# Kernel tuning notes

Measured on AMD Instinct MI355X. Metric: run time of the kernel, lower is better.

Reference implementation:

```python
import jax, jax.numpy as jnp
import numpy as np

DIM_Q = 512
DIM_K = 512
DIM_V = 512
NUM_HEADS = 8
LN_EPS = 1e-5


def setup_inputs() -> dict:
    key = jax.random.key(0)
    ks = jax.random.split(key, 12)
    s_q = 1.0 / np.sqrt(DIM_Q)
    s_k = 1.0 / np.sqrt(DIM_K)
    s_v = 1.0 / np.sqrt(DIM_V)
    return {
        "Q": jax.random.normal(ks[0], (8, 1024, DIM_Q), dtype=jnp.float32),
        "K": jax.random.normal(ks[1], (8, 1024, DIM_K), dtype=jnp.float32),
        "Wq": jax.random.uniform(ks[2], (DIM_Q, DIM_V), jnp.float32, -s_q, s_q),
        "bq": jax.random.uniform(ks[3], (DIM_V,), jnp.float32, -s_q, s_q),
        "Wk": jax.random.uniform(ks[4], (DIM_K, DIM_V), jnp.float32, -s_k, s_k),
        "bk": jax.random.uniform(ks[5], (DIM_V,), jnp.float32, -s_k, s_k),
        "Wv": jax.random.uniform(ks[6], (DIM_K, DIM_V), jnp.float32, -s_k, s_k),
        "bv": jax.random.uniform(ks[7], (DIM_V,), jnp.float32, -s_k, s_k),
        "Wo": jax.random.uniform(ks[8], (DIM_V, DIM_V), jnp.float32, -s_v, s_v),
        "bo": jax.random.uniform(ks[9], (DIM_V,), jnp.float32, -s_v, s_v),
        "g0": jnp.ones((DIM_V,), jnp.float32),
        "b0": jnp.zeros((DIM_V,), jnp.float32),
        "g1": jnp.ones((DIM_V,), jnp.float32),
        "b1": jnp.zeros((DIM_V,), jnp.float32),
    }


def _layer_norm(x, gamma, beta):
    mu = jnp.mean(x, axis=-1, keepdims=True)
    var = jnp.var(x, axis=-1, keepdims=True)
    return (x - mu) * jax.lax.rsqrt(var + LN_EPS) * gamma + beta


def reference(Q, K, Wq, bq, Wk, bk, Wv, bv, Wo, bo, g0, b0, g1, b1):
    B, Nq, _ = Q.shape
    Nk = K.shape[1]
    H = NUM_HEADS
    d = DIM_V // H  # head dim

    Qp = Q @ Wq + bq                      # [B, Nq, dim_V]
    Kp = K @ Wk + bk                      # [B, Nk, dim_V]
    Vp = K @ Wv + bv                      # [B, Nk, dim_V]

    Qh = Qp.reshape(B, Nq, H, d)
    Kh = Kp.reshape(B, Nk, H, d)
    Vh = Vp.reshape(B, Nk, H, d)

    scores = jnp.einsum("bqhd,bkhd->bhqk", Qh, Kh) / jnp.sqrt(jnp.float32(d))
    A = jax.nn.softmax(scores, axis=-1)   # [B, H, Nq, Nk]
    Oh = jnp.einsum("bhqk,bkhd->bqhd", A, Vh) + Qh  # residual with projected Q
    O = Oh.reshape(B, Nq, DIM_V)

    O = _layer_norm(O, g0, b0)
    O = O + jax.nn.relu(O @ Wo + bo)
    O = _layer_norm(O, g1, b1)
    return O
```

## Files before the change

kernel.cpp:

```cpp
#include <hip/hip_runtime.h>
#include <math.h>

#define DV 512
#define HD 64
#define NHEADS 8
#define SEQ 1024
#define NBATCH 8
#define MROWS (NBATCH * SEQ)

typedef __bf16 bf16;
typedef __bf16 bf16x8 __attribute__((ext_vector_type(8)));
typedef __bf16 bf16x4 __attribute__((ext_vector_type(4)));
typedef float f32x4 __attribute__((ext_vector_type(4)));

__device__ inline void gload_lds16(const void* g, void* l) {
  __builtin_amdgcn_global_load_lds(
      (const __attribute__((address_space(1))) unsigned int*)g,
      (__attribute__((address_space(3))) unsigned int*)l, 16, 0, 0);
}

__global__ __launch_bounds__(256) void prep_w(
    const float* __restrict__ W0, const float* __restrict__ W1,
    const float* __restrict__ W2, const float* __restrict__ W3,
    bf16* __restrict__ T0, bf16* __restrict__ T1,
    bf16* __restrict__ T2, bf16* __restrict__ T3)
{
  const int z = blockIdx.z;
  const float* W = z == 0 ? W0 : z == 1 ? W1 : z == 2 ? W2 : W3;
  bf16* WT = z == 0 ? T0 : z == 1 ? T1 : z == 2 ? T2 : T3;
  __shared__ float T[64][65];
  const int t = threadIdx.x;
  const int k0 = (blockIdx.x >> 3) * 64, n0 = (blockIdx.x & 7) * 64;
#pragma unroll
  for (int p = 0; p < 4; ++p) {
    int r = p * 16 + (t >> 4), c = (t & 15) * 4;
    float4 v = *(const float4*)&W[(size_t)(k0 + r) * DV + n0 + c];
    T[r][c] = v.x; T[r][c + 1] = v.y; T[r][c + 2] = v.z; T[r][c + 3] = v.w;
  }
  __syncthreads();
#pragma unroll
  for (int p = 0; p < 2; ++p) {
    int n = p * 32 + (t >> 3), kc = (t & 7) * 8;
    bf16x8 o;
#pragma unroll
    for (int j = 0; j < 8; ++j) o[j] = (bf16)T[kc + j][n];
    *(bf16x8*)&WT[(size_t)(n0 + n) * DV + k0 + kc] = o;
  }
}

template<bool AF, bool BF>
__device__ __forceinline__ void proj_core(
    const float* Af, const bf16* Ab, const float* Bf, const bf16* Bb,
    bf16* As, bf16* Bs, int m0, int n0, f32x4 (*acc)[4])
{
  const int tid = threadIdx.x;
  const int lane = tid & 63, w = tid >> 6;
  const int wm = w >> 1, wn = w & 1;
  const int cl = lane & 15, qd = lane >> 4;

  size_t offA[4], offB[4];
  int uOff[4], sOff[4];
#pragma unroll
  for (int t = 0; t < 4; ++t) {
    int S = t * 256 + tid;
    int row = S >> 3, kq = (S & 7) ^ (row & 7);
    offA[t] = (size_t)(m0 + row) * DV + kq * 8;
    offB[t] = (size_t)(n0 + row) * DV + kq * 8;
    uOff[t] = (t * 256 + w * 64) * 8;
    sOff[t] = S * 8;
  }

  float4 ra0[4], ra1[4], rb0[4], rb1[4];

#pragma unroll
  for (int t = 0; t < 4; ++t) {
    if (AF) {
      ra0[t] = *(const float4*)(Af + offA[t]);
      ra1[t] = *(const float4*)(Af + offA[t] + 4);
      bf16x8 o;
      o[0]=(bf16)ra0[t].x; o[1]=(bf16)ra0[t].y; o[2]=(bf16)ra0[t].z; o[3]=(bf16)ra0[t].w;
      o[4]=(bf16)ra1[t].x; o[5]=(bf16)ra1[t].y; o[6]=(bf16)ra1[t].z; o[7]=(bf16)ra1[t].w;
      *(bf16x8*)(As + sOff[t]) = o;
    } else {
      gload_lds16(Ab + offA[t], As + uOff[t]);
    }
    if (BF) {
      rb0[t] = *(const float4*)(Bf + offB[t]);
      rb1[t] = *(const float4*)(Bf + offB[t] + 4);
      bf16x8 o;
      o[0]=(bf16)rb0[t].x; o[1]=(bf16)rb0[t].y; o[2]=(bf16)rb0[t].z; o[3]=(bf16)rb0[t].w;
      o[4]=(bf16)rb1[t].x; o[5]=(bf16)rb1[t].y; o[6]=(bf16)rb1[t].z; o[7]=(bf16)rb1[t].w;
      *(bf16x8*)(Bs + sOff[t]) = o;
    } else {
      gload_lds16(Bb + offB[t], Bs + uOff[t]);
    }
  }

  for (int it = 0; it < 8; ++it) {
    __syncthreads();
    const int cur = it & 1;
    const int nb = (cur ^ 1) * 8192;
    const bool has = (it + 1 < 8);
    const size_t k0n = (size_t)(it + 1) * 64;
    if (has) {
#pragma unroll
      for (int t = 0; t < 4; ++t) {
        if (AF) { ra0[t] = *(const float4*)(Af + k0n + offA[t]);
                  ra1[t] = *(const float4*)(Af + k0n + offA[t] + 4); }
        else    gload_lds16(Ab + k0n + offA[t], As + nb + uOff[t]);
        if (BF) { rb0[t] = *(const float4*)(Bf + k0n + offB[t]);
                  rb1[t] = *(const float4*)(Bf + k0n + offB[t] + 4); }
        else    gload_lds16(Bb + k0n + offB[t], Bs + nb + uOff[t]);
      }
    }
    const bf16* A_ = As + cur * 8192;
    const bf16* B_ = Bs + cur * 8192;
#pragma unroll
    for (int cc = 0; cc < 2; ++cc) {
      bf16x8 af[4], bfr[4];
#pragma unroll
      for (int mi = 0; mi < 4; ++mi) {
        int row = wm * 64 + mi * 16 + cl;
        int slot = row * 8 + ((cc * 4 + qd) ^ (row & 7));
        af[mi] = *(const bf16x8*)(A_ + (size_t)slot * 8);
      }
#pragma unroll
      for (int ni = 0; ni < 4; ++ni) {
        int row = wn * 64 + ni * 16 + cl;
        int slot = row * 8 + ((cc * 4 + qd) ^ (row & 7));
        bfr[ni] = *(const bf16x8*)(B_ + (size_t)slot * 8);
      }
#pragma unroll
      for (int mi = 0; mi < 4; ++mi)
#pragma unroll
        for (int ni = 0; ni < 4; ++ni)
          acc[mi][ni] = __builtin_amdgcn_mfma_f32_16x16x32_bf16(
              af[mi], bfr[ni], acc[mi][ni], 0, 0, 0);
    }
    if (has) {
#pragma unroll
      for (int t = 0; t < 4; ++t) {
        if (AF) {
          bf16x8 o;
          o[0]=(bf16)ra0[t].x; o[1]=(bf16)ra0[t].y; o[2]=(bf16)ra0[t].z; o[3]=(bf16)ra0[t].w;
          o[4]=(bf16)ra1[t].x; o[5]=(bf16)ra1[t].y; o[6]=(bf16)ra1[t].z; o[7]=(bf16)ra1[t].w;
          *(bf16x8*)(As + nb + sOff[t]) = o;
        }
        if (BF) {
          bf16x8 o;
          o[0]=(bf16)rb0[t].x; o[1]=(bf16)rb0[t].y; o[2]=(bf16)rb0[t].z; o[3]=(bf16)rb0[t].w;
          o[4]=(bf16)rb1[t].x; o[5]=(bf16)rb1[t].y; o[6]=(bf16)rb1[t].z; o[7]=(bf16)rb1[t].w;
          *(bf16x8*)(Bs + nb + sOff[t]) = o;
        }
      }
    }
  }
}

__global__ __launch_bounds__(256) void gemm_proj(
    const float* __restrict__ Qf, const float* __restrict__ Kf,
    const bf16* __restrict__ WqT, const bf16* __restrict__ WkT,
    const bf16* __restrict__ WvT,
    const float* __restrict__ bq, const float* __restrict__ bk,
    const float* __restrict__ bv,
    bf16* __restrict__ Qp, bf16* __restrict__ Kp, bf16* __restrict__ VpT)
{
  __shared__ bf16 As[2 * 8192];
  __shared__ bf16 Bs[2 * 8192];
  const int z = blockIdx.z;
  int bx, by, N;
  if (z < 2) { by = blockIdx.x & 63; bx = blockIdx.x >> 6; N = DV; }
  else       { bx = blockIdx.x & 63; by = blockIdx.x >> 6; N = MROWS; }
  const int m0 = by * 128, n0 = bx * 128;

  f32x4 acc[4][4] = {};
  const float* bias;
  bf16* C;
  if (z == 0) { proj_core<true,  false>(Qf, nullptr, nullptr, WqT, As, Bs, m0, n0, acc); bias = bq; C = Qp; }
  else if (z == 1) { proj_core<true,  false>(Kf, nullptr, nullptr, WkT, As, Bs, m0, n0, acc); bias = bk; C = Kp; }
  else { proj_core<false, true>(nullptr, WvT, Kf, nullptr, As, Bs, m0, n0, acc); bias = bv; C = VpT; }

  const int lane = threadIdx.x & 63, w = threadIdx.x >> 6;
  const int wm = w >> 1, wn = w & 1;
  const int cl = lane & 15, qd = lane >> 4;
  float bcol[4] = {0.f, 0.f, 0.f, 0.f};
  if (z < 2)
#pragma unroll
    for (int ni = 0; ni < 4; ++ni) bcol[ni] = bias[n0 + wn * 64 + ni * 16 + cl];
#pragma unroll
  for (int mi = 0; mi < 4; ++mi)
#pragma unroll
    for (int r = 0; r < 4; ++r) {
      int gm = m0 + wm * 64 + mi * 16 + qd * 4 + r;
      float brow = (z == 2) ? bias[gm] : 0.f;
#pragma unroll
      for (int ni = 0; ni < 4; ++ni) {
        int gn = n0 + wn * 64 + ni * 16 + cl;
        float v = acc[mi][ni][r] + (z == 2 ? brow : bcol[ni]);
        C[(size_t)gm * N + gn] = (bf16)v;
      }
    }
}

__global__ __launch_bounds__(256) void attn_mfma(
    const bf16* __restrict__ Qp, const bf16* __restrict__ Kp,
    const bf16* __restrict__ VpT, bf16* __restrict__ Orb)
{
  __shared__ bf16 Ks[2][64 * 64];
  __shared__ bf16 Vs[2][64 * 64];
  __shared__ bf16 Ps[4][32 * 72];

  const int tid = threadIdx.x, lane = tid & 63, w = tid >> 6;
  const int cl = lane & 15, qd = lane >> 4;
  const int bh = blockIdx.x, b = bh >> 3, h = bh & 7;
  const int q0w = blockIdx.y * 128 + w * 32;

  const float SCL = 0.18033688011112042f;
  bf16x8 qa[2][2];
#pragma unroll
  for (int qt = 0; qt < 2; ++qt)
#pragma unroll
    for (int ch = 0; ch < 2; ++ch) {
      bf16x8 v = *(const bf16x8*)(Qp + ((size_t)b * SEQ + q0w + qt * 16 + cl) * DV
                                  + h * HD + ch * 32 + qd * 8);
#pragma unroll
      for (int j = 0; j < 8; ++j) v[j] = (bf16)((float)v[j] * SCL);
      qa[qt][ch] = v;
    }

  f32x4 o[4][2] = {};
  float lrun[2] = {0.f, 0.f};

  const bf16* Kbase = Kp + (size_t)b * SEQ * DV + h * HD;
  const bf16* Vbase = VpT + (size_t)h * HD * MROWS + (size_t)b * SEQ;
  bf16* Pw = &Ps[w][0];

  const int Sa = tid, Sb = 256 + tid;
  const int kRowA = Sa >> 3, kDgA = (Sa & 7) ^ (kRowA & 7);
  const int kRowB = Sb >> 3, kDgB = (Sb & 7) ^ (kRowB & 7);
  const size_t kOffA = (size_t)kRowA * DV + kDgA * 8;
  const size_t kOffB = (size_t)kRowB * DV + kDgB * 8;
  const size_t vOffA = (size_t)kRowA * MROWS + kDgA * 8;
  const size_t vOffB = (size_t)kRowB * MROWS + kDgB * 8;

  gload_lds16(Kbase + kOffA, &Ks[0][(size_t)(w * 64) * 8]);
  gload_lds16(Kbase + kOffB, &Ks[0][(size_t)(256 + w * 64) * 8]);
  gload_lds16(Vbase + vOffA, &Vs[0][(size_t)(w * 64) * 8]);
  gload_lds16(Vbase + vOffB, &Vs[0][(size_t)(256 + w * 64) * 8]);

  for (int it = 0; it < SEQ / 64; ++it) {
    __syncthreads();
    const int cur = it & 1;
    if (it + 1 < SEQ / 64) {
      const size_t kt = (size_t)(it + 1) * 64;
      gload_lds16(Kbase + kt * DV + kOffA, &Ks[cur ^ 1][(size_t)(w * 64) * 8]);
      gload_lds16(Kbase + kt * DV + kOffB, &Ks[cur ^ 1][(size_t)(256 + w * 64) * 8]);
      gload_lds16(Vbase + kt + vOffA, &Vs[cur ^ 1][(size_t)(w * 64) * 8]);
      gload_lds16(Vbase + kt + vOffB, &Vs[cur ^ 1][(size_t)(256 + w * 64) * 8]);
    }
    const bf16* K_ = &Ks[cur][0];
    const bf16* V_ = &Vs[cur][0];

    f32x4 sc[4][2] = {};
#pragma unroll
    for (int ch = 0; ch < 2; ++ch) {
      bf16x8 kf[4];
#pragma unroll
      for (int kt4 = 0; kt4 < 4; ++kt4) {
        int key = kt4 * 16 + cl;
        int slot = key * 8 + ((ch * 4 + qd) ^ (key & 7));
        kf[kt4] = *(const bf16x8*)(K_ + (size_t)slot * 8);
      }
#pragma unroll
      for (int kt4 = 0; kt4 < 4; ++kt4)
#pragma unroll
        for (int qt = 0; qt < 2; ++qt)
          sc[kt4][qt] = __builtin_amdgcn_mfma_f32_16x16x32_bf16(
              kf[kt4], qa[qt][ch], sc[kt4][qt], 0, 0, 0);
    }

#pragma unroll
    for (int qt = 0; qt < 2; ++qt) {
      float sum = 0.f;
#pragma unroll
      for (int kt4 = 0; kt4 < 4; ++kt4) {
        float p0 = __builtin_amdgcn_exp2f(sc[kt4][qt][0]);
        float p1 = __builtin_amdgcn_exp2f(sc[kt4][qt][1]);
        float p2 = __builtin_amdgcn_exp2f(sc[kt4][qt][2]);
        float p3 = __builtin_amdgcn_exp2f(sc[kt4][qt][3]);
        sum += (p0 + p1) + (p2 + p3);
        bf16x4 pk;
        pk[0] = (bf16)p0; pk[1] = (bf16)p1; pk[2] = (bf16)p2; pk[3] = (bf16)p3;
        *(bf16x4*)(Pw + (size_t)(qt * 16 + cl) * 72 + kt4 * 16 + qd * 4) = pk;
      }
      sum += __shfl_xor(sum, 16);
      sum += __shfl_xor(sum, 32);
      lrun[qt] += sum;
    }

#pragma unroll
    for (int kc = 0; kc < 2; ++kc) {
      bf16x8 pb[2];
#pragma unroll
      for (int qt = 0; qt < 2; ++qt)
        pb[qt] = *(const bf16x8*)(Pw + (size_t)(qt * 16 + cl) * 72 + kc * 32 + qd * 8);
#pragma unroll
      for (int dt = 0; dt < 4; ++dt) {
        int d = dt * 16 + cl;
        int slot = d * 8 + ((kc * 4 + qd) ^ (d & 7));
        bf16x8 vf = *(const bf16x8*)(V_ + (size_t)slot * 8);
#pragma unroll
        for (int qt = 0; qt < 2; ++qt)
          o[dt][qt] = __builtin_amdgcn_mfma_f32_16x16x32_bf16(
              vf, pb[qt], o[dt][qt], 0, 0, 0);
      }
    }
  }

#pragma unroll
  for (int qt = 0; qt < 2; ++qt) {
    float inv = 1.f / lrun[qt];
    size_t rowoff = ((size_t)b * SEQ + q0w + qt * 16 + cl) * DV + h * HD;
#pragma unroll
    for (int dt = 0; dt < 4; ++dt) {
      bf16x4 rv = *(const bf16x4*)(Qp + rowoff + dt * 16 + qd * 4);
      bf16x4 st;
      st[0] = (bf16)(o[dt][qt][0] * inv + (float)rv[0]);
      st[1] = (bf16)(o[dt][qt][1] * inv + (float)rv[1]);
      st[2] = (bf16)(o[dt][qt][2] * inv + (float)rv[2]);
      st[3] = (bf16)(o[dt][qt][3] * inv + (float)rv[3]);
      *(bf16x4*)(Orb + rowoff + dt * 16 + qd * 4) = st;
    }
  }
}

__global__ __launch_bounds__(256) void gemm_fused(
    const bf16* __restrict__ Orb, const bf16* __restrict__ WoT,
    const float* __restrict__ bo,
    const float* __restrict__ g0, const float* __restrict__ b0,
    const float* __restrict__ g1, const float* __restrict__ b1,
    float* __restrict__ out)
{
  __shared__ bf16 Bsm[32 * 512];
  __shared__ bf16 As[2][2048 * 8];
  const int tid = threadIdx.x, lane = tid & 63, w = tid >> 6;
  const int cl = lane & 15, qd = lane >> 4;
  const int m0 = blockIdx.x * 32;

  size_t offA[8];
  int uOff[8];
#pragma unroll
  for (int t = 0; t < 8; ++t) {
    int S = t * 256 + tid;
    int frow = S >> 2, kq = (S & 3) ^ ((frow >> 1) & 3);
    offA[t] = (size_t)frow * DV + kq * 8;
    uOff[t] = (t * 256 + w * 64) * 8;
  }

#pragma unroll
  for (int t = 0; t < 8; ++t)
    gload_lds16(WoT + offA[t], As[0] + uOff[t]);

  {
    const int q = tid >> 3, c0 = (tid & 7) * 64;
    const bf16* src = Orb + (size_t)(m0 + q) * DV + c0;
    float x[64];
    float s = 0.f, s2 = 0.f;
#pragma unroll
    for (int j = 0; j < 8; ++j) {
      bf16x8 xv = *(const bf16x8*)(src + j * 8);
#pragma unroll
      for (int e = 0; e < 8; ++e) {
        float f = (float)xv[e];
        x[j * 8 + e] = f; s += f; s2 += f * f;
      }
    }
    s  += __shfl_xor(s, 1);  s  += __shfl_xor(s, 2);  s  += __shfl_xor(s, 4);
    s2 += __shfl_xor(s2, 1); s2 += __shfl_xor(s2, 2); s2 += __shfl_xor(s2, 4);
    float mu = s * (1.f / DV);
    float inv = rsqrtf(s2 * (1.f / DV) - mu * mu + 1e-5f);
#pragma unroll
    for (int j = 0; j < 8; ++j) {
      float4 ga = *(const float4*)(g0 + c0 + j * 8);
      float4 gb = *(const float4*)(g0 + c0 + j * 8 + 4);
      float4 ba = *(const float4*)(b0 + c0 + j * 8);
      float4 bb = *(const float4*)(b0 + c0 + j * 8 + 4);
      bf16x8 o;
      o[0] = (bf16)((x[j*8+0] - mu) * inv * ga.x + ba.x);
      o[1] = (bf16)((x[j*8+1] - mu) * inv * ga.y + ba.y);
      o[2] = (bf16)((x[j*8+2] - mu) * inv * ga.z + ba.z);
      o[3] = (bf16)((x[j*8+3] - mu) * inv * ga.w + ba.w);
      o[4] = (bf16)((x[j*8+4] - mu) * inv * gb.x + bb.x);
      o[5] = (bf16)((x[j*8+5] - mu) * inv * gb.y + bb.y);
      o[6] = (bf16)((x[j*8+6] - mu) * inv * gb.z + bb.z);
      o[7] = (bf16)((x[j*8+7] - mu) * inv * gb.w + bb.w);
      int g = (tid & 7) * 8 + j;
      int slot = q * 64 + (g ^ (q & 7));
      *(bf16x8*)(Bsm + (size_t)slot * 8) = o;
    }
  }

  f32x4 acc[8][2] = {};
  for (int it = 0; it < 16; ++it) {
    __syncthreads();
    const int cur = it & 1;
    if (it + 1 < 16) {
#pragma unroll
      for (int t = 0; t < 8; ++t)
        gload_lds16(WoT + (size_t)(it + 1) * 32 + offA[t], As[cur ^ 1] + uOff[t]);
    }
    bf16x8 bfr[2];
#pragma unroll
    for (int nt = 0; nt < 2; ++nt) {
      int q = nt * 16 + cl;
      int slot = q * 64 + ((it * 4 + qd) ^ (q & 7));
      bfr[nt] = *(const bf16x8*)(Bsm + (size_t)slot * 8);
    }
#pragma unroll
    for (int mt = 0; mt < 8; ++mt) {
      int frow = (w * 8 + mt) * 16 + cl;
      int slot = frow * 4 + (qd ^ ((frow >> 1) & 3));
      bf16x8 af = *(const bf16x8*)(As[cur] + (size_t)slot * 8);
#pragma unroll
      for (int nt = 0; nt < 2; ++nt)
        acc[mt][nt] = __builtin_amdgcn_mfma_f32_16x16x32_bf16(
            af, bfr[nt], acc[mt][nt], 0, 0, 0);
    }
  }

  __syncthreads();
  float* red = (float*)As;
  float y[8][2][4];
  float sy[2], sy2[2];
#pragma unroll
  for (int nt = 0; nt < 2; ++nt) {
    sy[nt] = 0.f; sy2[nt] = 0.f;
    const int q = nt * 16 + cl;
#pragma unroll
    for (int mt = 0; mt < 8; ++mt) {
      const int f0 = (w * 8 + mt) * 16 + qd * 4;
      float4 bov = *(const float4*)(bo + f0);
      int g = f0 >> 3;
      int slot = q * 64 + (g ^ (q & 7));
      bf16x4 rv = *(const bf16x4*)(Bsm + (size_t)slot * 8 + (qd & 1) * 4);
      const float* bp = (const float*)&bov;
#pragma unroll
      for (int r = 0; r < 4; ++r) {
        float v = fmaxf(acc[mt][nt][r] + bp[r], 0.f) + (float)rv[r];
        y[mt][nt][r] = v;
        sy[nt] += v; sy2[nt] += v * v;
      }
    }
    sy[nt]  += __shfl_xor(sy[nt], 16);  sy[nt]  += __shfl_xor(sy[nt], 32);
    sy2[nt] += __shfl_xor(sy2[nt], 16); sy2[nt] += __shfl_xor(sy2[nt], 32);
  }
  if (qd == 0) {
#pragma unroll
    for (int nt = 0; nt < 2; ++nt) {
      int q = nt * 16 + cl;
      red[(q * 4 + w) * 2 + 0] = sy[nt];
      red[(q * 4 + w) * 2 + 1] = sy2[nt];
    }
  }
  __syncthreads();
#pragma unroll
  for (int nt = 0; nt < 2; ++nt) {
    const int q = nt * 16 + cl;
    float s = 0.f, s2 = 0.f;
#pragma unroll
    for (int ww = 0; ww < 4; ++ww) {
      s  += red[(q * 4 + ww) * 2 + 0];
      s2 += red[(q * 4 + ww) * 2 + 1];
    }
    float mu1 = s * (1.f / DV);
    float inv1 = rsqrtf(s2 * (1.f / DV) - mu1 * mu1 + 1e-5f);
    size_t rowoff = (size_t)(m0 + q) * DV;
#pragma unroll
    for (int mt = 0; mt < 8; ++mt) {
      const int f0 = (w * 8 + mt) * 16 + qd * 4;
      float4 gv = *(const float4*)(g1 + f0);
      float4 bv = *(const float4*)(b1 + f0);
      float4 ov;
      ov.x = (y[mt][nt][0] - mu1) * inv1 * gv.x + bv.x;
      ov.y = (y[mt][nt][1] - mu1) * inv1 * gv.y + bv.y;
      ov.z = (y[mt][nt][2] - mu1) * inv1 * gv.z + bv.z;
      ov.w = (y[mt][nt][3] - mu1) * inv1 * gv.w + bv.w;
      *(float4*)(out + rowoff + f0) = ov;
    }
  }
}

extern "C" void kernel_launch(void* const* d_in, const int* in_sizes, int n_in,
                              void* d_out, int out_size, void* d_ws, size_t ws_size,
                              hipStream_t stream)
{
  const float* Q  = (const float*)d_in[0];
  const float* Kf = (const float*)d_in[1];
  const float* Wq = (const float*)d_in[2];
  const float* bq = (const float*)d_in[3];
  const float* Wk = (const float*)d_in[4];
  const float* bk = (const float*)d_in[5];
  const float* Wv = (const float*)d_in[6];
  const float* bv = (const float*)d_in[7];
  const float* Wo = (const float*)d_in[8];
  const float* bo = (const float*)d_in[9];
  const float* g0 = (const float*)d_in[10];
  const float* b0 = (const float*)d_in[11];
  const float* g1 = (const float*)d_in[12];
  const float* b1 = (const float*)d_in[13];
  float* out = (float*)d_out;

  const size_t MB = 1ull << 20;
  char* W = (char*)d_ws;
  bf16* Orb = (bf16*)(W + 0);
  bf16* Qp  = (bf16*)(W + 8 * MB);
  bf16* Kp  = (bf16*)(W + 16 * MB);
  bf16* VpT = (bf16*)(W + 24 * MB);
  bf16* WqT = (bf16*)(W + 32 * MB);
  bf16* WkT = (bf16*)(W + 32 * MB + 512 * 1024);
  bf16* WvT = (bf16*)(W + 33 * MB);
  bf16* WoT = (bf16*)(W + 33 * MB + 512 * 1024);

  dim3 blk(256);
  prep_w<<<dim3(64, 1, 4), blk, 0, stream>>>(Wq, Wk, Wv, Wo, WqT, WkT, WvT, WoT);
  gemm_proj<<<dim3(256, 1, 3), blk, 0, stream>>>(
      Q, Kf, WqT, WkT, WvT, bq, bk, bv, Qp, Kp, VpT);
  attn_mfma<<<dim3(NBATCH * NHEADS, SEQ / 128), blk, 0, stream>>>(Qp, Kp, VpT, Orb);
  gemm_fused<<<dim3(MROWS / 32), blk, 0, stream>>>(
      Orb, WoT, bo, g0, b0, g1, b1, out);
}
```

Measured before the change: 185.2 us.

## Load GEMM operands directly from global into registers, bypassing LDS staging

The projection GEMM and the output-projection GEMM no longer stage A/B tiles through double-buffered LDS with barriers. Each lane instead loads its MFMA fragments straight from global memory into registers, prefetching the next K slice one step ahead. This removes LDS traffic and per-iteration __syncthreads, and lets the fused LN kernel keep only a small reduction buffer in shared memory. The cost is that operands are no longer shared across waves, so each wave re-reads overlapping rows from global/L2 with less coalesced access.

After: 225.3 us. +21.6%, slower.

```diff
diff --git a/kernel.cpp b/kernel.cpp
--- a/kernel.cpp
+++ b/kernel.cpp
@@ -17,6 +17,13 @@
   __builtin_amdgcn_global_load_lds(
       (const __attribute__((address_space(1))) unsigned int*)g,
       (__attribute__((address_space(3))) unsigned int*)l, 16, 0, 0);
+}
+
+__device__ __forceinline__ bf16x8 cvt8(float4 a, float4 b) {
+  bf16x8 o;
+  o[0] = (bf16)a.x; o[1] = (bf16)a.y; o[2] = (bf16)a.z; o[3] = (bf16)a.w;
+  o[4] = (bf16)b.x; o[5] = (bf16)b.y; o[6] = (bf16)b.z; o[7] = (bf16)b.w;
+  return o;
 }
 
 __global__ __launch_bounds__(256) void prep_w(
@@ -48,115 +55,6 @@
   }
 }
 
-template<bool AF, bool BF>
-__device__ __forceinline__ void proj_core(
-    const float* Af, const bf16* Ab, const float* Bf, const bf16* Bb,
-    bf16* As, bf16* Bs, int m0, int n0, f32x4 (*acc)[4])
-{
-  const int tid = threadIdx.x;
-  const int lane = tid & 63, w = tid >> 6;
-  const int wm = w >> 1, wn = w & 1;
-  const int cl = lane & 15, qd = lane >> 4;
-
-  size_t offA[4], offB[4];
-  int uOff[4], sOff[4];
-#pragma unroll
-  for (int t = 0; t < 4; ++t) {
-    int S = t * 256 + tid;
-    int row = S >> 3, kq = (S & 7) ^ (row & 7);
-    offA[t] = (size_t)(m0 + row) * DV + kq * 8;
-    offB[t] = (size_t)(n0 + row) * DV + kq * 8;
-    uOff[t] = (t * 256 + w * 64) * 8;
-    sOff[t] = S * 8;
-  }
-
-  float4 ra0[4], ra1[4], rb0[4], rb1[4];
-
-#pragma unroll
-  for (int t = 0; t < 4; ++t) {
-    if (AF) {
-      ra0[t] = *(const float4*)(Af + offA[t]);
-      ra1[t] = *(const float4*)(Af + offA[t] + 4);
-      bf16x8 o;
-      o[0]=(bf16)ra0[t].x; o[1]=(bf16)ra0[t].y; o[2]=(bf16)ra0[t].z; o[3]=(bf16)ra0[t].w;
-      o[4]=(bf16)ra1[t].x; o[5]=(bf16)ra1[t].y; o[6]=(bf16)ra1[t].z; o[7]=(bf16)ra1[t].w;
-      *(bf16x8*)(As + sOff[t]) = o;
-    } else {
-      gload_lds16(Ab + offA[t], As + uOff[t]);
-    }
-    if (BF) {
-      rb0[t] = *(const float4*)(Bf + offB[t]);
-      rb1[t] = *(const float4*)(Bf + offB[t] + 4);
-      bf16x8 o;
-      o[0]=(bf16)rb0[t].x; o[1]=(bf16)rb0[t].y; o[2]=(bf16)rb0[t].z; o[3]=(bf16)rb0[t].w;
-      o[4]=(bf16)rb1[t].x; o[5]=(bf16)rb1[t].y; o[6]=(bf16)rb1[t].z; o[7]=(bf16)rb1[t].w;
-      *(bf16x8*)(Bs + sOff[t]) = o;
-    } else {
-      gload_lds16(Bb + offB[t], Bs + uOff[t]);
-    }
-  }
-
-  for (int it = 0; it < 8; ++it) {
-    __syncthreads();
-    const int cur = it & 1;
-    const int nb = (cur ^ 1) * 8192;
-    const bool has = (it + 1 < 8);
-    const size_t k0n = (size_t)(it + 1) * 64;
-    if (has) {
-#pragma unroll
-      for (int t = 0; t < 4; ++t) {
-        if (AF) { ra0[t] = *(const float4*)(Af + k0n + offA[t]);
-                  ra1[t] = *(const float4*)(Af + k0n + offA[t] + 4); }
-        else    gload_lds16(Ab + k0n + offA[t], As + nb + uOff[t]);
-        if (BF) { rb0[t] = *(const float4*)(Bf + k0n + offB[t]);
-                  rb1[t] = *(const float4*)(Bf + k0n + offB[t] + 4); }
-        else    gload_lds16(Bb + k0n + offB[t], Bs + nb + uOff[t]);
-      }
-    }
-    const bf16* A_ = As + cur * 8192;
-    const bf16* B_ = Bs + cur * 8192;
-#pragma unroll
-    for (int cc = 0; cc < 2; ++cc) {
-      bf16x8 af[4], bfr[4];
-#pragma unroll
-      for (int mi = 0; mi < 4; ++mi) {
-        int row = wm * 64 + mi * 16 + cl;
-        int slot = row * 8 + ((cc * 4 + qd) ^ (row & 7));
-        af[mi] = *(const bf16x8*)(A_ + (size_t)slot * 8);
-      }
-#pragma unroll
-      for (int ni = 0; ni < 4; ++ni) {
-        int row = wn * 64 + ni * 16 + cl;
-        int slot = row * 8 + ((cc * 4 + qd) ^ (row & 7));
-        bfr[ni] = *(const bf16x8*)(B_ + (size_t)slot * 8);
-      }
-#pragma unroll
-      for (int mi = 0; mi < 4; ++mi)
-#pragma unroll
-        for (int ni = 0; ni < 4; ++ni)
-          acc[mi][ni] = __builtin_amdgcn_mfma_f32_16x16x32_bf16(
-              af[mi], bfr[ni], acc[mi][ni], 0, 0, 0);
-    }
-    if (has) {
-#pragma unroll
-      for (int t = 0; t < 4; ++t) {
-        if (AF) {
-          bf16x8 o;
-          o[0]=(bf16)ra0[t].x; o[1]=(bf16)ra0[t].y; o[2]=(bf16)ra0[t].z; o[3]=(bf16)ra0[t].w;
-          o[4]=(bf16)ra1[t].x; o[5]=(bf16)ra1[t].y; o[6]=(bf16)ra1[t].z; o[7]=(bf16)ra1[t].w;
-          *(bf16x8*)(As + nb + sOff[t]) = o;
-        }
-        if (BF) {
-          bf16x8 o;
-          o[0]=(bf16)rb0[t].x; o[1]=(bf16)rb0[t].y; o[2]=(bf16)rb0[t].z; o[3]=(bf16)rb0[t].w;
-          o[4]=(bf16)rb1[t].x; o[5]=(bf16)rb1[t].y; o[6]=(bf16)rb1[t].z; o[7]=(bf16)rb1[t].w;
-          *(bf16x8*)(Bs + nb + sOff[t]) = o;
-        }
-      }
-    }
-  }
-}
-
 __global__ __launch_bounds__(256) void gemm_proj(
     const float* __restrict__ Qf, const float* __restrict__ Kf,
     const bf16* __restrict__ WqT, const bf16* __restrict__ WkT,
@@ -165,24 +63,117 @@
     const float* __restrict__ bv,
     bf16* __restrict__ Qp, bf16* __restrict__ Kp, bf16* __restrict__ VpT)
 {
-  __shared__ bf16 As[2 * 8192];
-  __shared__ bf16 Bs[2 * 8192];
   const int z = blockIdx.z;
   int bx, by, N;
   if (z < 2) { by = blockIdx.x & 63; bx = blockIdx.x >> 6; N = DV; }
   else       { bx = blockIdx.x & 63; by = blockIdx.x >> 6; N = MROWS; }
   const int m0 = by * 128, n0 = bx * 128;
-
-  f32x4 acc[4][4] = {};
-  const float* bias;
-  bf16* C;
-  if (z == 0) { proj_core<true,  false>(Qf, nullptr, nullptr, WqT, As, Bs, m0, n0, acc); bias = bq; C = Qp; }
-  else if (z == 1) { proj_core<true,  false>(Kf, nullptr, nullptr, WkT, As, Bs, m0, n0, acc); bias = bk; C = Kp; }
-  else { proj_core<false, true>(nullptr, WvT, Kf, nullptr, As, Bs, m0, n0, acc); bias = bv; C = VpT; }
-
   const int lane = threadIdx.x & 63, w = threadIdx.x >> 6;
   const int wm = w >> 1, wn = w & 1;
   const int cl = lane & 15, qd = lane >> 4;
+
+  f32x4 acc[4][4] = {};
+
+  if (z < 2) {
+    const float* A = z ? Kf : Qf;
+    const bf16*  B = z ? WkT : WqT;
+    const float* Ap[4];
+    const bf16* Bp[4];
+#pragma unroll
+    for (int mi = 0; mi < 4; ++mi)
+      Ap[mi] = A + (size_t)(m0 + wm * 64 + mi * 16 + cl) * DV + qd * 8;
+#pragma unroll
+    for (int ni = 0; ni < 4; ++ni)
+      Bp[ni] = B + (size_t)(n0 + wn * 64 + ni * 16 + cl) * DV + qd * 8;
+
+    float4 fa[4][2]; bf16x8 cb[4];
+#pragma unroll
+    for (int mi = 0; mi < 4; ++mi) {
+      fa[mi][0] = *(const float4*)Ap[mi];
+      fa[mi][1] = *(const float4*)(Ap[mi] + 4);
+    }
+#pragma unroll
+    for (int ni = 0; ni < 4; ++ni) cb[ni] = *(const bf16x8*)Bp[ni];
+
+    for (int it = 0; it < 16; ++it) {
+      float4 na[4][2]; bf16x8 nb[4];
+      if (it + 1 < 16) {
+        const int k = (it + 1) * 32;
+#pragma unroll
+        for (int mi = 0; mi < 4; ++mi) {
+          na[mi][0] = *(const float4*)(Ap[mi] + k);
+          na[mi][1] = *(const float4*)(Ap[mi] + k + 4);
+        }
+#pragma unroll
+        for (int ni = 0; ni < 4; ++ni) nb[ni] = *(const bf16x8*)(Bp[ni] + k);
+      }
+      bf16x8 af[4];
+#pragma unroll
+      for (int mi = 0; mi < 4; ++mi) af[mi] = cvt8(fa[mi][0], fa[mi][1]);
+#pragma unroll
+      for (int mi = 0; mi < 4; ++mi)
+#pragma unroll
+        for (int ni = 0; ni < 4; ++ni)
+          acc[mi][ni] = __builtin_amdgcn_mfma_f32_16x16x32_bf16(
+              af[mi], cb[ni], acc[mi][ni], 0, 0, 0);
+      if (it + 1 < 16) {
+#pragma unroll
+        for (int mi = 0; mi < 4; ++mi) { fa[mi][0] = na[mi][0]; fa[mi][1] = na[mi][1]; }
+#pragma unroll
+        for (int ni = 0; ni < 4; ++ni) cb[ni] = nb[ni];
+      }
+    }
+  } else {
+    const bf16* Ap[4];
+    const float* Bp[4];
+#pragma unroll
+    for (int mi = 0; mi < 4; ++mi)
+      Ap[mi] = WvT + (size_t)(m0 + wm * 64 + mi * 16 + cl) * DV + qd * 8;
+#pragma unroll
+    for (int ni = 0; ni < 4; ++ni)
+      Bp[ni] = Kf + (size_t)(n0 + wn * 64 + ni * 16 + cl) * DV + qd * 8;
+
+    bf16x8 ca[4]; float4 fb[4][2];
+#pragma unroll
+    for (int mi = 0; mi < 4; ++mi) ca[mi] = *(const bf16x8*)Ap[mi];
+#pragma unroll
+    for (int ni = 0; ni < 4; ++ni) {
+      fb[ni][0] = *(const float4*)Bp[ni];
+      fb[ni][1] = *(const float4*)(Bp[ni] + 4);
+    }
+
+    for (int it = 0; it < 16; ++it) {
+      bf16x8 na[4]; float4 nb[4][2];
+      if (it + 1 < 16) {
+        const int k = (it + 1) * 32;
+#pragma unroll
+        for (int mi = 0; mi < 4; ++mi) na[mi] = *(const bf16x8*)(Ap[mi] + k);
+#pragma unroll
+        for (int ni = 0; ni < 4; ++ni) {
+          nb[ni][0] = *(const float4*)(Bp[ni] + k);
+          nb[ni][1] = *(const float4*)(Bp[ni] + k + 4);
+        }
+      }
+      bf16x8 bfm[4];
+#pragma unroll
+      for (int ni = 0; ni < 4; ++ni) bfm[ni] = cvt8(fb[ni][0], fb[ni][1]);
+#pragma unroll
+      for (int mi = 0; mi < 4; ++mi)
+#pragma unroll
+        for (int ni = 0; ni < 4; ++ni)
+          acc[mi][ni] = __builtin_amdgcn_mfma_f32_16x16x32_bf16(
+              ca[mi], bfm[ni], acc[mi][ni], 0, 0, 0);
+      if (it + 1 < 16) {
+#pragma unroll
+        for (int mi = 0; mi < 4; ++mi) ca[mi] = na[mi];
+#pragma unroll
+        for (int ni = 0; ni < 4; ++ni) { fb[ni][0] = nb[ni][0]; fb[ni][1] = nb[ni][1]; }
+      }
+    }
+  }
+
+  const float* bias = z == 0 ? bq : z == 1 ? bk : bv;
+  bf16* C = z == 0 ? Qp : z == 1 ? Kp : VpT;
   float bcol[4] = {0.f, 0.f, 0.f, 0.f};
   if (z < 2)
 #pragma unroll
@@ -342,24 +333,10 @@
     float* __restrict__ out)
 {
   __shared__ bf16 Bsm[32 * 512];
-  __shared__ bf16 As[2][2048 * 8];
+  __shared__ float red[32 * 4 * 2];
   const int tid = threadIdx.x, lane = tid & 63, w = tid >> 6;
   const int cl = lane & 15, qd = lane >> 4;
   const int m0 = blockIdx.x * 32;
-
-  size_t offA[8];
-  int uOff[8];
-#pragma unroll
-  for (int t = 0; t < 8; ++t) {
-    int S = t * 256 + tid;
-    int frow = S >> 2, kq = (S & 3) ^ ((frow >> 1) & 3);
-    offA[t] = (size_t)frow * DV + kq * 8;
-    uOff[t] = (t * 256 + w * 64) * 8;
-  }
-
-#pragma unroll
-  for (int t = 0; t < 8; ++t)
-    gload_lds16(WoT + offA[t], As[0] + uOff[t]);
 
   {
     const int q = tid >> 3, c0 = (tid & 7) * 64;
@@ -399,15 +376,24 @@
       *(bf16x8*)(Bsm + (size_t)slot * 8) = o;
     }
   }
+  __syncthreads();
+
+  const bf16* Ap[8];
+#pragma unroll
+  for (int mt = 0; mt < 8; ++mt)
+    Ap[mt] = WoT + (size_t)((w * 8 + mt) * 16 + cl) * DV + qd * 8;
+
+  bf16x8 caf[8];
+#pragma unroll
+  for (int mt = 0; mt < 8; ++mt) caf[mt] = *(const bf16x8*)Ap[mt];
 
   f32x4 acc[8][2] = {};
   for (int it = 0; it < 16; ++it) {
-    __syncthreads();
-    const int cur = it & 1;
+    bf16x8 naf[8];
     if (it + 1 < 16) {
-#pragma unroll
-      for (int t = 0; t < 8; ++t)
-        gload_lds16(WoT + (size_t)(it + 1) * 32 + offA[t], As[cur ^ 1] + uOff[t]);
+      const int k = (it + 1) * 32;
+#pragma unroll
+      for (int mt = 0; mt < 8; ++mt) naf[mt] = *(const bf16x8*)(Ap[mt] + k);
     }
     bf16x8 bfr[2];
 #pragma unroll
@@ -417,19 +403,16 @@
       bfr[nt] = *(const bf16x8*)(Bsm + (size_t)slot * 8);
     }
 #pragma unroll
-    for (int mt = 0; mt < 8; ++mt) {
-      int frow = (w * 8 + mt) * 16 + cl;
-      int slot = frow * 4 + (qd ^ ((frow >> 1) & 3));
-      bf16x8 af = *(const bf16x8*)(As[cur] + (size_t)slot * 8);
+    for (int mt = 0; mt < 8; ++mt)
 #pragma unroll
       for (int nt = 0; nt < 2; ++nt)
         acc[mt][nt] = __builtin_amdgcn_mfma_f32_16x16x32_bf16(
-            af, bfr[nt], acc[mt][nt], 0, 0, 0);
-    }
-  }
-
-  __syncthreads();
-  float* red = (float*)As;
+            caf[mt], bfr[nt], acc[mt][nt], 0, 0, 0);
+    if (it + 1 < 16)
+#pragma unroll
+      for (int mt = 0; mt < 8; ++mt) caf[mt] = naf[mt];
+  }
+
   float y[8][2][4];
   float sy[2], sy2[2];
 #pragma unroll
```

## Load bf16 weight fragments straight into registers, stage only activations in LDS

Applied to the files above, without the earlier changes.

The projection GEMM core stops staging the pre-transposed bf16 weight tile through LDS. Each wave now reads its weight MFMA fragments directly from global memory into registers, double-buffered across k-steps, and only the fp32 activation tile is converted and written to shared memory. This halves LDS usage and removes the LDS reads for the weight operand. In exchange it adds global loads that may be redundantly fetched by waves sharing columns, and more registers are held live.

Measured after the change: 192.7 us. 4.0% more time.

```diff
diff --git a/kernel.cpp b/kernel.cpp
--- a/kernel.cpp
+++ b/kernel.cpp
@@ -17,6 +17,13 @@
   __builtin_amdgcn_global_load_lds(
       (const __attribute__((address_space(1))) unsigned int*)g,
       (__attribute__((address_space(3))) unsigned int*)l, 16, 0, 0);
+}
+
+__device__ __forceinline__ bf16x8 cvt8(float4 a, float4 b) {
+  bf16x8 o;
+  o[0] = (bf16)a.x; o[1] = (bf16)a.y; o[2] = (bf16)a.z; o[3] = (bf16)a.w;
+  o[4] = (bf16)b.x; o[5] = (bf16)b.y; o[6] = (bf16)b.z; o[7] = (bf16)b.w;
+  return o;
 }
 
 __global__ __launch_bounds__(256) void prep_w(
@@ -48,111 +55,97 @@
   }
 }
 
-template<bool AF, bool BF>
+template<bool SA>
 __device__ __forceinline__ void proj_core(
-    const float* Af, const bf16* Ab, const float* Bf, const bf16* Bb,
-    bf16* As, bf16* Bs, int m0, int n0, f32x4 (*acc)[4])
+    const float* __restrict__ Sg, const bf16* __restrict__ Wg,
+    int s0, int w0, bf16* Ss, f32x4 (*acc)[4])
 {
   const int tid = threadIdx.x;
   const int lane = tid & 63, w = tid >> 6;
   const int wm = w >> 1, wn = w & 1;
   const int cl = lane & 15, qd = lane >> 4;
-
-  size_t offA[4], offB[4];
-  int uOff[4], sOff[4];
+  const int sw = SA ? wm : wn;
+  const int ww = SA ? wn : wm;
+
+  size_t offS[4];
+  int sOff[4];
 #pragma unroll
   for (int t = 0; t < 4; ++t) {
     int S = t * 256 + tid;
     int row = S >> 3, kq = (S & 7) ^ (row & 7);
-    offA[t] = (size_t)(m0 + row) * DV + kq * 8;
-    offB[t] = (size_t)(n0 + row) * DV + kq * 8;
-    uOff[t] = (t * 256 + w * 64) * 8;
+    offS[t] = (size_t)(s0 + row) * DV + kq * 8;
     sOff[t] = S * 8;
   }
 
-  float4 ra0[4], ra1[4], rb0[4], rb1[4];
-
+  const bf16* Wp[4];
+#pragma unroll
+  for (int i = 0; i < 4; ++i)
+    Wp[i] = Wg + (size_t)(w0 + ww * 64 + i * 16 + cl) * DV + qd * 8;
+
+  float4 r0[4], r1[4];
 #pragma unroll
   for (int t = 0; t < 4; ++t) {
-    if (AF) {
-      ra0[t] = *(const float4*)(Af + offA[t]);
-      ra1[t] = *(const float4*)(Af + offA[t] + 4);
-      bf16x8 o;
-      o[0]=(bf16)ra0[t].x; o[1]=(bf16)ra0[t].y; o[2]=(bf16)ra0[t].z; o[3]=(bf16)ra0[t].w;
-      o[4]=(bf16)ra1[t].x; o[5]=(bf16)ra1[t].y; o[6]=(bf16)ra1[t].z; o[7]=(bf16)ra1[t].w;
-      *(bf16x8*)(As + sOff[t]) = o;
-    } else {
-      gload_lds16(Ab + offA[t], As + uOff[t]);
-    }
-    if (BF) {
-      rb0[t] = *(const float4*)(Bf + offB[t]);
-      rb1[t] = *(const float4*)(Bf + offB[t] + 4);
-      bf16x8 o;
-      o[0]=(bf16)rb0[t].x; o[1]=(bf16)rb0[t].y; o[2]=(bf16)rb0[t].z; o[3]=(bf16)rb0[t].w;
-      o[4]=(bf16)rb1[t].x; o[5]=(bf16)rb1[t].y; o[6]=(bf16)rb1[t].z; o[7]=(bf16)rb1[t].w;
-      *(bf16x8*)(Bs + sOff[t]) = o;
-    } else {
-      gload_lds16(Bb + offB[t], Bs + uOff[t]);
-    }
-  }
+    r0[t] = *(const float4*)(Sg + offS[t]);
+    r1[t] = *(const float4*)(Sg + offS[t] + 4);
+  }
+#pragma unroll
+  for (int t = 0; t < 4; ++t) *(bf16x8*)(Ss + sOff[t]) = cvt8(r0[t], r1[t]);
+
+  bf16x8 wcur[4][2], wnext[4][2];
+#pragma unroll
+  for (int i = 0; i < 4; ++i)
+#pragma unroll
+    for (int cc = 0; cc < 2; ++cc)
+      wcur[i][cc] = *(const bf16x8*)(Wp[i] + cc * 32);
 
   for (int it = 0; it < 8; ++it) {
     __syncthreads();
     const int cur = it & 1;
     const int nb = (cur ^ 1) * 8192;
     const bool has = (it + 1 < 8);
-    const size_t k0n = (size_t)(it + 1) * 64;
     if (has) {
+      const size_t kn = (size_t)(it + 1) * 64;
 #pragma unroll
       for (int t = 0; t < 4; ++t) {
-        if (AF) { ra0[t] = *(const float4*)(Af + k0n + offA[t]);
-                  ra1[t] = *(const float4*)(Af + k0n + offA[t] + 4); }
-        else    gload_lds16(Ab + k0n + offA[t], As + nb + uOff[t]);
-        if (BF) { rb0[t] = *(const float4*)(Bf + k0n + offB[t]);
-                  rb1[t] = *(const float4*)(Bf + k0n + offB[t] + 4); }
-        else    gload_lds16(Bb + k0n + offB[t], Bs + nb + uOff[t]);
-      }
-    }
-    const bf16* A_ = As + cur * 8192;
-    const bf16* B_ = Bs + cur * 8192;
+        r0[t] = *(const float4*)(Sg + kn + offS[t]);
+        r1[t] = *(const float4*)(Sg + kn + offS[t] + 4);
+      }
+#pragma unroll
+      for (int i = 0; i < 4; ++i)
+#pragma unroll
+        for (int cc = 0; cc < 2; ++cc)
+          wnext[i][cc] = *(const bf16x8*)(Wp[i] + kn + cc * 32);
+    }
+    const bf16* S_ = Ss + cur * 8192;
 #pragma unroll
     for (int cc = 0; cc < 2; ++cc) {
-      bf16x8 af[4], bfr[4];
-#pragma unroll
-      for (int mi = 0; mi < 4; ++mi) {
-        int row = wm * 64 + mi * 16 + cl;
+      bf16x8 sf[4];
+#pragma unroll
+      for (int j = 0; j < 4; ++j) {
+        int row = sw * 64 + j * 16 + cl;
         int slot = row * 8 + ((cc * 4 + qd) ^ (row & 7));
-        af[mi] = *(const bf16x8*)(A_ + (size_t)slot * 8);
-      }
-#pragma unroll
-      for (int ni = 0; ni < 4; ++ni) {
-        int row = wn * 64 + ni * 16 + cl;
-        int slot = row * 8 + ((cc * 4 + qd) ^ (row & 7));
-        bfr[ni] = *(const bf16x8*)(B_ + (size_t)slot * 8);
+        sf[j] = *(const bf16x8*)(S_ + (size_t)slot * 8);
       }
 #pragma unroll
       for (int mi = 0; mi < 4; ++mi)
 #pragma unroll
-        for (int ni = 0; ni < 4; ++ni)
-          acc[mi][ni] = __builtin_amdgcn_mfma_f32_16x16x32_bf16(
-              af[mi], bfr[ni], acc[mi][ni], 0, 0, 0);
+        for (int ni = 0; ni < 4; ++ni) {
+          if (SA)
+            acc[mi][ni] = __builtin_amdgcn_mfma_f32_16x16x32_bf16(
+                sf[mi], wcur[ni][cc], acc[mi][ni], 0, 0, 0);
+          else
+            acc[mi][ni] = __builtin_amdgcn_mfma_f32_16x16x32_bf16(
+                wcur[mi][cc], sf[ni], acc[mi][ni], 0, 0, 0);
+        }
     }
     if (has) {
 #pragma unroll
-      for (int t = 0; t < 4; ++t) {
-        if (AF) {
-          bf16x8 o;
-          o[0]=(bf16)ra0[t].x; o[1]=(bf16)ra0[t].y; o[2]=(bf16)ra0[t].z; o[3]=(bf16)ra0[t].w;
-          o[4]=(bf16)ra1[t].x; o[5]=(bf16)ra1[t].y; o[6]=(bf16)ra1[t].z; o[7]=(bf16)ra1[t].w;
-          *(bf16x8*)(As + nb + sOff[t]) = o;
-        }
-        if (BF) {
-          bf16x8 o;
-          o[0]=(bf16)rb0[t].x; o[1]=(bf16)rb0[t].y; o[2]=(bf16)rb0[t].z; o[3]=(bf16)rb0[t].w;
-          o[4]=(bf16)rb1[t].x; o[5]=(bf16)rb1[t].y; o[6]=(bf16)rb1[t].z; o[7]=(bf16)rb1[t].w;
-          *(bf16x8*)(Bs + nb + sOff[t]) = o;
-        }
-      }
+      for (int t = 0; t < 4; ++t)
+        *(bf16x8*)(Ss + nb + sOff[t]) = cvt8(r0[t], r1[t]);
+#pragma unroll
+      for (int i = 0; i < 4; ++i)
+#pragma unroll
+        for (int cc = 0; cc < 2; ++cc) wcur[i][cc] = wnext[i][cc];
     }
   }
 }
@@ -165,21 +158,20 @@
     const float* __restrict__ bv,
     bf16* __restrict__ Qp, bf16* __restrict__ Kp, bf16* __restrict__ VpT)
 {
-  __shared__ bf16 As[2 * 8192];
-  __shared__ bf16 Bs[2 * 8192];
+  __shared__ bf16 Ss[2 * 8192];
   const int z = blockIdx.z;
-  int bx, by, N;
-  if (z < 2) { by = blockIdx.x & 63; bx = blockIdx.x >> 6; N = DV; }
-  else       { bx = blockIdx.x & 63; by = blockIdx.x >> 6; N = MROWS; }
-  const int m0 = by * 128, n0 = bx * 128;
-
+  int m0, n0, N;
   f32x4 acc[4][4] = {};
-  const float* bias;
-  bf16* C;
-  if (z == 0) { proj_core<true,  false>(Qf, nullptr, nullptr, WqT, As, Bs, m0, n0, acc); bias = bq; C = Qp; }
-  else if (z == 1) { proj_core<true,  false>(Kf, nullptr, nullptr, WkT, As, Bs, m0, n0, acc); bias = bk; C = Kp; }
-  else { proj_core<false, true>(nullptr, WvT, Kf, nullptr, As, Bs, m0, n0, acc); bias = bv; C = VpT; }
-
+  if (z < 2) {
+    m0 = (blockIdx.x & 63) * 128; n0 = (blockIdx.x >> 6) * 128; N = DV;
+    proj_core<true>(z ? Kf : Qf, z ? WkT : WqT, m0, n0, Ss, acc);
+  } else {
+    n0 = (blockIdx.x & 63) * 128; m0 = (blockIdx.x >> 6) * 128; N = MROWS;
+    proj_core<false>(Kf, WvT, n0, m0, Ss, acc);
+  }
+
+  const float* bias = z == 0 ? bq : z == 1 ? bk : bv;
+  bf16* C = z == 0 ? Qp : z == 1 ? Kp : VpT;
   const int lane = threadIdx.x & 63, w = threadIdx.x >> 6;
   const int wm = w >> 1, wn = w & 1;
   const int cl = lane & 15, qd = lane >> 4;
```
